# Kernel tuning notes

Measured on AMD Instinct MI355X. Metric: run time of the kernel, lower is better.

The kernel has to match this reference:

```python
import jax, jax.numpy as jnp
import numpy as np

BL = 512
Q_DIM = K_DIM = V_DIM = 512
R = 2
C = Q_DIM // R  # 256


def setup_inputs() -> dict:
    key = jax.random.key(0)
    ks = jax.random.split(key, 11)
    L = 32768
    x1 = jax.random.normal(ks[0], (1, Q_DIM, L), dtype=jnp.float32)
    x2 = jax.random.normal(ks[1], (1, Q_DIM, L), dtype=jnp.float32)
    mask = jnp.ones((1, 1, L), dtype=jnp.float32)
    s_in = 1.0 / np.sqrt(Q_DIM)
    s_out = 1.0 / np.sqrt(C)
    Wq = jax.random.normal(ks[2], (C, Q_DIM), dtype=jnp.float32) * s_in
    bq = jax.random.normal(ks[3], (C,), dtype=jnp.float32) * 0.01
    Wk = jax.random.normal(ks[4], (C, K_DIM), dtype=jnp.float32) * s_in
    bk = jax.random.normal(ks[5], (C,), dtype=jnp.float32) * 0.01
    Wv = jax.random.normal(ks[6], (C, V_DIM), dtype=jnp.float32) * s_in
    bv = jax.random.normal(ks[7], (C,), dtype=jnp.float32) * 0.01
    Wo = jax.random.normal(ks[8], (V_DIM, C), dtype=jnp.float32) * s_out
    bo = jax.random.normal(ks[9], (V_DIM,), dtype=jnp.float32) * 0.01
    return {"x1": x1, "x2": x2, "mask": mask, "Wq": Wq, "bq": bq,
            "Wk": Wk, "bk": bk, "Wv": Wv, "bv": bv, "Wo": Wo, "bo": bo}


def _sliding_att(x1, mask, Wq, bq, Wk, bk, Wv, bv, Wo, bo):
    bl = BL
    half = bl // 2
    B, _, L = x1.shape  # B == 1 (asserted in original)
    # 1x1 Conv1d projections == per-position matmuls over channels
    q = jnp.einsum('oc,bcl->bol', Wq, x1) + bq[None, :, None]  # (1,C,L)
    k = jnp.einsum('oc,bcl->bol', Wk, x1) + bk[None, :, None]
    v = jnp.einsum('oc,bcl->bol', Wv, x1) + bv[None, :, None]
    c1 = q.shape[1]
    nb = L // bl  # L chosen as multiple of bl; padding branch is a no-op
    pm = mask[:, 0:1, :]  # (1,1,L)
    # query blocks: (nb, C, bl)
    qb = q.reshape(1, c1, nb, bl).transpose(0, 2, 1, 3).reshape(nb, c1, bl)
    # pad K/V/mask with bl//2 zeros each side, gather overlapping windows of width 2*bl
    k_pad = jnp.pad(k, ((0, 0), (0, 0), (half, half)))[0]      # (C, L+bl)
    v_pad = jnp.pad(v, ((0, 0), (0, 0), (half, half)))[0]
    pm_pad = jnp.pad(pm, ((0, 0), (0, 0), (half, half)))[0, 0]  # (L+bl,)
    idx = jnp.arange(nb)[:, None] * bl + jnp.arange(2 * bl)[None, :]  # (nb, 2bl)
    kw = k_pad[:, idx].transpose(1, 0, 2)  # (nb, C, 2bl)
    vw = v_pad[:, idx].transpose(1, 0, 2)  # (nb, C, 2bl)
    pmw = pm_pad[idx][:, None, :]          # (nb, 1, 2bl)
    # banded window mask: query i attends keys j with i <= j < i+bl (in window coords)
    rows = jnp.arange(bl)[:, None]
    cols = jnp.arange(2 * bl)[None, :]
    wmask = ((cols >= rows) & (cols < rows + bl)).astype(x1.dtype)  # (bl, 2bl)
    fmask = wmask[None, :, :] * pmw  # (nb, bl, 2bl)
    scale = 1.0 / np.sqrt(c1)
    energy = jnp.einsum('ncl,ncm->nlm', qb, kw) * scale  # (nb, bl, 2bl)
    attn = jax.nn.softmax(energy + jnp.log(fmask + 1e-6), axis=-1) * fmask
    out = jnp.einsum('ncm,nlm->ncl', vw, attn)  # (nb, C, bl)
    out = jax.nn.relu(out)
    out = jnp.einsum('oc,ncl->nol', Wo, out) + bo[None, :, None]  # (nb, V, bl)
    out = out[None].transpose(0, 2, 1, 3).reshape(1, Wo.shape[0], nb * bl)
    return out[:, :, :L] * pm


def reference(x1, x2, mask, Wq, bq, Wk, bk, Wv, bv, Wo, bo):
    # x2 is accepted by the original forward but unused in self-attention
    return _sliding_att(x1, mask, Wq, bq, Wk, bk, Wv, bv, Wo, bo)
```

## Files before the change

kernel.cpp:

```cpp
#include <hip/hip_runtime.h>
#include <hip/hip_bf16.h>
#include <math.h>

#define L 32768
#define C 256
#define QD 512
#define SCALE (1.0f/16.0f)

typedef __hip_bfloat16 bf16;
typedef short v8s __attribute__((ext_vector_type(8)));
typedef short v4s __attribute__((ext_vector_type(4)));
typedef float v4f __attribute__((ext_vector_type(4)));

__device__ __forceinline__ void ldst16(void* lds, const void* g) {
    __builtin_amdgcn_global_load_lds(
        (const __attribute__((address_space(1))) unsigned int*)g,
        (__attribute__((address_space(3))) unsigned int*)lds, 16, 0, 0);
}
__device__ __forceinline__ short bfbits(float x) {
    bf16 h = __float2bfloat16(x);
    return *reinterpret_cast<short*>(&h);
}

__global__ __launch_bounds__(256) void prep(
    const float* __restrict__ Wq, const float* __restrict__ Wk,
    const float* __restrict__ Wv, const float* __restrict__ bq,
    const float* __restrict__ bk, const float* __restrict__ bv,
    const float* __restrict__ Wo,
    bf16* __restrict__ Wall, bf16* __restrict__ Wob, float* __restrict__ ball)
{
    int i = blockIdx.x * 256 + threadIdx.x;
    if (i < 768*512) {
        int row = i >> 9, idx = i & 511;
        const float* src = row < 256 ? Wq : row < 512 ? Wk : Wv;
        Wall[i] = __float2bfloat16(src[(row & 255) * 512 + idx]);
    } else if (i < 768*512 + 512*256) {
        int j = i - 768*512;
        Wob[j] = __float2bfloat16(Wo[j]);
    } else if (i < 768*512 + 512*256 + 768) {
        int j = i - 768*512 - 512*256;
        ball[j] = j < 256 ? bq[j] : j < 512 ? bk[j - 256] : bv[j - 512];
    }
}

__global__ __launch_bounds__(256) void convt(
    const float* __restrict__ x, short* __restrict__ xT)
{
    __shared__ short st[64*72];
    const int t = threadIdx.x;
    const int l0 = blockIdx.x * 64, c0 = blockIdx.y * 64;
    #pragma unroll
    for (int i = 0; i < 2; i++) {
        int v = i*256 + t;
        int c = v >> 3, l8 = (v & 7) << 3;
        const float* p = x + (size_t)(c0 + c) * L + l0 + l8;
        float4 f0 = *(const float4*)p;
        float4 f1 = *(const float4*)(p + 4);
        bf16* stb = (bf16*)st;
        stb[(l8+0)*72 + c] = __float2bfloat16(f0.x);
        stb[(l8+1)*72 + c] = __float2bfloat16(f0.y);
        stb[(l8+2)*72 + c] = __float2bfloat16(f0.z);
        stb[(l8+3)*72 + c] = __float2bfloat16(f0.w);
        stb[(l8+4)*72 + c] = __float2bfloat16(f1.x);
        stb[(l8+5)*72 + c] = __float2bfloat16(f1.y);
        stb[(l8+6)*72 + c] = __float2bfloat16(f1.z);
        stb[(l8+7)*72 + c] = __float2bfloat16(f1.w);
    }
    __syncthreads();
    #pragma unroll
    for (int i = 0; i < 2; i++) {
        int v = i*256 + t;
        int l = v >> 3, c8 = (v & 7) << 3;
        *(v8s*)(xT + (size_t)(l0 + l) * QD + c0 + c8) = *(const v8s*)&st[l*72 + c8];
    }
}

__global__ __launch_bounds__(256) void qkv_gemm(
    const bf16* __restrict__ A, const bf16* __restrict__ B,
    const float* __restrict__ ball,
    bf16* __restrict__ qT, bf16* __restrict__ kT, bf16* __restrict__ vB)
{
    __shared__ short sA[128*32];
    __shared__ short sB[128*32];
    __shared__ short sE[128*136];

    const int t    = threadIdx.x;
    const int lane = t & 63;
    const int w    = t >> 6;
    const int wm   = w & 1, wn = w >> 1;
    const int col  = lane & 15, quad = lane >> 4;
    const int n0   = blockIdx.x * 128;
    const int my   = blockIdx.y;
    const int m0   = my * 128;

    v4f acc[4][4];
    #pragma unroll
    for (int i = 0; i < 4; i++)
        #pragma unroll
        for (int j = 0; j < 4; j++) acc[i][j] = (v4f){0.f,0.f,0.f,0.f};

    for (int k0 = 0; k0 < QD; k0 += 32) {
        #pragma unroll
        for (int j = 0; j < 2; j++) {
            int idx = j*256 + t;
            int m = idx >> 2, k8 = (idx & 3) << 3;
            ldst16(&sA[idx*8], A + (size_t)(m0 + m) * QD + k0 + k8);
        }
        #pragma unroll
        for (int j = 0; j < 2; j++) {
            int idx = j*256 + t;
            int n = idx >> 2, k8 = (idx & 3) << 3;
            ldst16(&sB[idx*8], B + (size_t)(n0 + n) * QD + k0 + k8);
        }
        __syncthreads();
        v8s af[4], bf[4];
        #pragma unroll
        for (int mt = 0; mt < 4; mt++)
            af[mt] = *(const v8s*)&sA[(wm*64 + mt*16 + col)*32 + quad*8];
        #pragma unroll
        for (int nt = 0; nt < 4; nt++)
            bf[nt] = *(const v8s*)&sB[(wn*64 + nt*16 + col)*32 + quad*8];
        #pragma unroll
        for (int mt = 0; mt < 4; mt++)
            #pragma unroll
            for (int nt = 0; nt < 4; nt++)
                acc[mt][nt] = __builtin_amdgcn_mfma_f32_16x16x32_bf16(af[mt], bf[nt], acc[mt][nt], 0, 0, 0);
        __syncthreads();
    }

    float bias_v[4][4];
    #pragma unroll
    for (int mt = 0; mt < 4; mt++)
        #pragma unroll
        for (int r = 0; r < 4; r++)
            bias_v[mt][r] = ball[m0 + wm*64 + mt*16 + quad*4 + r];

    bf16* sEb = (bf16*)sE;
    if (my < 4) {
        #pragma unroll
        for (int mt = 0; mt < 4; mt++)
            #pragma unroll
            for (int nt = 0; nt < 4; nt++)
                #pragma unroll
                for (int r = 0; r < 4; r++)
                    sEb[(wn*64 + nt*16 + col)*136 + wm*64 + mt*16 + quad*4 + r] =
                        __float2bfloat16(acc[mt][nt][r] + bias_v[mt][r]);
        __syncthreads();
        bf16* dst = (my < 2) ? qT : kT;
        const int c0 = (my & 1) * 128;
        #pragma unroll
        for (int j = 0; j < 8; j++) {
            int idx = j*256 + t;
            int n = idx >> 4, c8 = (idx & 15) << 3;
            *(v8s*)(dst + (size_t)(n0 + n) * C + c0 + c8) = *(const v8s*)&sE[n*136 + c8];
        }
    } else {
        #pragma unroll
        for (int mt = 0; mt < 4; mt++)
            #pragma unroll
            for (int nt = 0; nt < 4; nt++)
                #pragma unroll
                for (int r = 0; r < 4; r++)
                    sEb[(wm*64 + mt*16 + quad*4 + r)*136 + wn*64 + nt*16 + col] =
                        __float2bfloat16(acc[mt][nt][r] + bias_v[mt][r]);
        __syncthreads();
        const int c0 = (my - 4) * 128;
        #pragma unroll
        for (int j = 0; j < 8; j++) {
            int idx = j*256 + t;
            int m = idx >> 4, n8 = (idx & 15) << 3;
            *(v8s*)(vB + (size_t)(c0 + m) * L + n0 + n8) = *(const v8s*)&sE[m*136 + n8];
        }
    }
}

__global__ __launch_bounds__(256) void out_gemm(
    const bf16* __restrict__ A, const bf16* __restrict__ B,
    const float* __restrict__ bo, const float* __restrict__ mask,
    float* __restrict__ out)
{
    __shared__ short sA[128*32];
    __shared__ short sB[128*32];
    __shared__ float sEf[64*132];

    const int t    = threadIdx.x;
    const int lane = t & 63;
    const int w    = t >> 6;
    const int wm   = w & 1, wn = w >> 1;
    const int col  = lane & 15, quad = lane >> 4;
    const int n0   = blockIdx.x * 128;
    const int m0   = blockIdx.y * 128;

    v4f acc[4][4];
    #pragma unroll
    for (int i = 0; i < 4; i++)
        #pragma unroll
        for (int j = 0; j < 4; j++) acc[i][j] = (v4f){0.f,0.f,0.f,0.f};

    for (int k0 = 0; k0 < C; k0 += 32) {
        #pragma unroll
        for (int j = 0; j < 2; j++) {
            int idx = j*256 + t;
            int m = idx >> 2, k8 = (idx & 3) << 3;
            ldst16(&sA[idx*8], A + (size_t)(m0 + m) * C + k0 + k8);
        }
        #pragma unroll
        for (int j = 0; j < 2; j++) {
            int idx = j*256 + t;
            int n = idx >> 2, k8 = (idx & 3) << 3;
            ldst16(&sB[idx*8], B + (size_t)(n0 + n) * C + k0 + k8);
        }
        __syncthreads();
        v8s af[4], bf[4];
        #pragma unroll
        for (int mt = 0; mt < 4; mt++)
            af[mt] = *(const v8s*)&sA[(wm*64 + mt*16 + col)*32 + quad*8];
        #pragma unroll
        for (int nt = 0; nt < 4; nt++)
            bf[nt] = *(const v8s*)&sB[(wn*64 + nt*16 + col)*32 + quad*8];
        #pragma unroll
        for (int mt = 0; mt < 4; mt++)
            #pragma unroll
            for (int nt = 0; nt < 4; nt++)
                acc[mt][nt] = __builtin_amdgcn_mfma_f32_16x16x32_bf16(af[mt], bf[nt], acc[mt][nt], 0, 0, 0);
        __syncthreads();
    }

    #pragma unroll
    for (int half = 0; half < 2; half++) {
        if (wm == half) {
            #pragma unroll
            for (int mt = 0; mt < 4; mt++) {
                #pragma unroll
                for (int r = 0; r < 4; r++) {
                    float bb = bo[m0 + half*64 + mt*16 + quad*4 + r];
                    #pragma unroll
                    for (int nt = 0; nt < 4; nt++)
                        sEf[(mt*16 + quad*4 + r)*132 + wn*64 + nt*16 + col] =
                            acc[mt][nt][r] + bb;
                }
            }
        }
        __syncthreads();
        #pragma unroll
        for (int j = 0; j < 8; j++) {
            int idx = j*256 + t;
            int row = idx >> 5, s4 = (idx & 31) << 2;
            float4 vv = *(const float4*)&sEf[row*132 + s4];
            float4 mk = *(const float4*)&mask[n0 + s4];
            vv.x *= mk.x; vv.y *= mk.y; vv.z *= mk.z; vv.w *= mk.w;
            *(float4*)&out[(size_t)(m0 + half*64 + row) * L + n0 + s4] = vv;
        }
        __syncthreads();
    }
}

__device__ __forceinline__ void load_chunk(
    const short* __restrict__ kT, const short* __restrict__ vB,
    int a0, int t, v8s kreg[4], v8s vreg[4])
{
    #pragma unroll
    for (int j = 0; j < 4; j++) {
        int idx = j*512 + t;
        int r = idx >> 5, s = idx & 31;
        int a = min(max(a0 + r, 0), L - 1);
        kreg[j] = *(const v8s*)(kT + (size_t)a * C + s*8);
    }
    #pragma unroll
    for (int j = 0; j < 4; j++) {
        int idx = j*512 + t;
        int c = idx >> 3, s = idx & 7;
        int ab = min(max(a0 + s*8, 0), L - 8);
        vreg[j] = *(const v8s*)(vB + (size_t)c * L + ab);
    }
}

__device__ __forceinline__ void store_chunk(
    short* __restrict__ sK, short* __restrict__ sVt, int t,
    const v8s kreg[4], const v8s vreg[4])
{
    #pragma unroll
    for (int j = 0; j < 4; j++) {
        int idx = j*512 + t;
        int r = idx >> 5, s = idx & 31;
        *(v8s*)&sK[r*264 + s*8] = kreg[j];
    }
    #pragma unroll
    for (int j = 0; j < 4; j++) {
        int idx = j*512 + t;
        int c = idx >> 3, s = idx & 7;
        *(v8s*)&sVt[c*72 + s*8] = vreg[j];
    }
}

__global__ __launch_bounds__(512, 1) void attn_mfma(
    const bf16* __restrict__ qT, const bf16* __restrict__ kT,
    const bf16* __restrict__ vB, const float* __restrict__ mask,
    bf16* __restrict__ aoT)
{
    __shared__ short sK [2][64*264];
    __shared__ short sVt[2][256*72];
    __shared__ short sP [8][16*72];

    const int t    = threadIdx.x;
    const int w    = t >> 6;
    const int lane = t & 63;
    const int col  = lane & 15;
    const int quad = lane >> 4;
    const int bx   = blockIdx.x;
    const int tile = ((bx & 7) << 5) | (bx >> 3);
    const int p0   = tile * 128;
    const int abase = p0 - 256;

    v8s qf[8];
    {
        const short* qp = (const short*)qT + (size_t)(p0 + w*16 + col) * C + quad*8;
        #pragma unroll
        for (int ks = 0; ks < 8; ks++) qf[ks] = *(const v8s*)(qp + ks*32);
    }

    v4f oacc[16];
    #pragma unroll
    for (int i = 0; i < 16; i++) oacc[i] = (v4f){0.f, 0.f, 0.f, 0.f};
    float mrow[4] = {-1e30f, -1e30f, -1e30f, -1e30f};
    float lrow[4] = {0.f, 0.f, 0.f, 0.f};

    const short* kTs = (const short*)kT;
    const short* vBs = (const short*)vB;
    bf16* sPw  = (bf16*)sP[w];
    const short* sPws = (const short*)sP[w];

    v8s kreg[4], vreg[4];
    load_chunk(kTs, vBs, abase, t, kreg, vreg);
    store_chunk(sK[0], sVt[0], t, kreg, vreg);
    __syncthreads();

    for (int ch = 0; ch < 10; ch++) {
        const int a0  = abase + ch*64;
        const int cur = ch & 1;
        const bool pf = (ch < 9);
        if (pf)
            load_chunk(kTs, vBs, a0 + 64, t, kreg, vreg);

        v4f e[4];
        #pragma unroll
        for (int nt = 0; nt < 4; nt++) {
            v4f acc = {0.f, 0.f, 0.f, 0.f};
            const short* kp = &sK[cur][(nt*16 + col)*264 + quad*8];
            #pragma unroll
            for (int ks = 0; ks < 8; ks++) {
                v8s bfrag = *(const v8s*)(kp + ks*32);
                acc = __builtin_amdgcn_mfma_f32_16x16x32_bf16(qf[ks], bfrag, acc, 0, 0, 0);
            }
            e[nt] = acc;
        }

        float cmax[4] = {-1e30f, -1e30f, -1e30f, -1e30f};
        #pragma unroll
        for (int nt = 0; nt < 4; nt++) {
            int a  = a0 + nt*16 + col;
            int aa = ch*64 + nt*16 + col;
            float mval = (a >= 0 && a < L) ? mask[a] : 0.f;
            #pragma unroll
            for (int r = 0; r < 4; r++) {
                int rel = aa - (w*16 + quad*4 + r);
                bool valid = ((unsigned)rel < 512u) && (mval > 0.f);
                float ev = valid ? e[nt][r] * SCALE : -1e30f;
                e[nt][r] = ev;
                cmax[r] = fmaxf(cmax[r], ev);
            }
        }
        #pragma unroll
        for (int off = 1; off < 16; off <<= 1) {
            #pragma unroll
            for (int r = 0; r < 4; r++)
                cmax[r] = fmaxf(cmax[r], __shfl_xor(cmax[r], off));
        }

        float alpha[4];
        #pragma unroll
        for (int r = 0; r < 4; r++) {
            float mnew = fmaxf(mrow[r], cmax[r]);
            alpha[r] = __expf(mrow[r] - mnew);
            mrow[r] = mnew;
        }

        float psum[4] = {0.f, 0.f, 0.f, 0.f};
        #pragma unroll
        for (int nt = 0; nt < 4; nt++) {
            #pragma unroll
            for (int r = 0; r < 4; r++) {
                float ev = e[nt][r];
                float p = (ev > -9e29f) ? __expf(ev - mrow[r]) : 0.f;
                psum[r] += p;
                sPw[(quad*4 + r)*72 + nt*16 + col] = __float2bfloat16(p);
            }
        }
        #pragma unroll
        for (int off = 1; off < 16; off <<= 1) {
            #pragma unroll
            for (int r = 0; r < 4; r++)
                psum[r] += __shfl_xor(psum[r], off);
        }
        #pragma unroll
        for (int r = 0; r < 4; r++) lrow[r] = lrow[r]*alpha[r] + psum[r];

        {
            int src = (col >> 2) << 4;
            float a0b = __shfl(alpha[0], src);
            float a1b = __shfl(alpha[1], src);
            float a2b = __shfl(alpha[2], src);
            float a3b = __shfl(alpha[3], src);
            int rr = col & 3;
            float aO = (rr == 0) ? a0b : (rr == 1) ? a1b : (rr == 2) ? a2b : a3b;
            #pragma unroll
            for (int i = 0; i < 16; i++) {
                oacc[i][0] *= aO; oacc[i][1] *= aO;
                oacc[i][2] *= aO; oacc[i][3] *= aO;
            }
        }

        {
            v8s pf0 = *(const v8s*)&sPws[col*72 + quad*8];
            v8s pf1 = *(const v8s*)&sPws[col*72 + quad*8 + 32];
            #pragma unroll
            for (int ct = 0; ct < 16; ct++) {
                const short* vp = &sVt[cur][(ct*16 + col)*72 + quad*8];
                v8s vf0 = *(const v8s*)vp;
                v8s vf1 = *(const v8s*)(vp + 32);
                oacc[ct] = __builtin_amdgcn_mfma_f32_16x16x32_bf16(vf0, pf0, oacc[ct], 0, 0, 0);
                oacc[ct] = __builtin_amdgcn_mfma_f32_16x16x32_bf16(vf1, pf1, oacc[ct], 0, 0, 0);
            }
        }

        if (pf) {
            store_chunk(sK[cur ^ 1], sVt[cur ^ 1], t, kreg, vreg);
            __syncthreads();
        }
    }

    {
        int src = (col >> 2) << 4;
        float l0b = __shfl(lrow[0], src);
        float l1b = __shfl(lrow[1], src);
        float l2b = __shfl(lrow[2], src);
        float l3b = __shfl(lrow[3], src);
        int rr = col & 3;
        float lO = (rr == 0) ? l0b : (rr == 1) ? l1b : (rr == 2) ? l2b : l3b;
        float inv = (lO > 0.f) ? 1.f / lO : 0.f;
        const int qg = p0 + w*16 + col;
        short* aorow = (short*)aoT + (size_t)qg * C;
        #pragma unroll
        for (int ct = 0; ct < 16; ct++) {
            v4s pk;
            #pragma unroll
            for (int r = 0; r < 4; r++)
                pk[r] = bfbits(fmaxf(oacc[ct][r] * inv, 0.f));
            *(v4s*)(aorow + ct*16 + quad*4) = pk;
        }
    }
}

extern "C" void kernel_launch(void* const* d_in, const int* in_sizes, int n_in,
                              void* d_out, int out_size, void* d_ws, size_t ws_size,
                              hipStream_t stream)
{
    const float* x1   = (const float*)d_in[0];
    const float* mask = (const float*)d_in[2];
    const float* Wq   = (const float*)d_in[3];
    const float* bq   = (const float*)d_in[4];
    const float* Wk   = (const float*)d_in[5];
    const float* bk   = (const float*)d_in[6];
    const float* Wv   = (const float*)d_in[7];
    const float* bv   = (const float*)d_in[8];
    const float* Wo   = (const float*)d_in[9];
    const float* bo   = (const float*)d_in[10];
    float* out = (float*)d_out;

    bf16* x1T  = (bf16*)d_ws;
    bf16* Wall = x1T + (size_t)L * QD;
    bf16* Wob  = Wall + 768*512;
    float* ball = (float*)(Wob + 512*256);
    bf16* qT   = (bf16*)(ball + 768);
    bf16* kT   = qT + (size_t)L * C;
    bf16* vB   = kT + (size_t)L * C;
    bf16* aoT  = vB + (size_t)L * C;

    dim3 blk(256);
    prep<<<dim3((768*512 + 512*256 + 768 + 255)/256), blk, 0, stream>>>(
        Wq, Wk, Wv, bq, bk, bv, Wo, Wall, Wob, ball);
    convt<<<dim3(L/64, QD/64), blk, 0, stream>>>(x1, (short*)x1T);
    qkv_gemm<<<dim3(L/128, 6), blk, 0, stream>>>(Wall, x1T, ball, qT, kT, vB);
    attn_mfma<<<dim3(L/128), dim3(512), 0, stream>>>(qT, kT, vB, mask, aoT);
    out_gemm<<<dim3(L/128, 4), blk, 0, stream>>>(Wob, aoT, bo, mask, out);
}
```

Measured before the change: 292.7 us.

## Transpose QK^T so probabilities stay in registers and drop LDS double buffering

Swaps the MFMA operand order so each lane holds one query column, which puts the softmax row statistics in a single scalar per lane. The bf16 probabilities are then fed straight from registers into 16x16x16 MFMAs for the PV product, with no shared-memory P staging. The K/V double buffer and its register prefetch are replaced by a single buffer loaded synchronously between two barriers. This frees LDS and registers so the launch bound can target 4 blocks per CU. The cost is that global loads are no longer overlapped with compute inside a block, so latency hiding depends on the other resident blocks.

```diff
diff --git a/kernel.cpp b/kernel.cpp
--- a/kernel.cpp
+++ b/kernel.cpp
@@ -20,6 +20,10 @@
 __device__ __forceinline__ short bfbits(float x) {
     bf16 h = __float2bfloat16(x);
     return *reinterpret_cast<short*>(&h);
+}
+__device__ __forceinline__ v4f mfma16(v4s a, v4s b, v4f c) {
+    asm("v_mfma_f32_16x16x16_bf16 %0, %1, %2, %0" : "+v"(c) : "v"(a), "v"(b));
+    return c;
 }
 
 __global__ __launch_bounds__(256) void prep(
@@ -255,52 +259,47 @@
     }
 }
 
-__device__ __forceinline__ void load_chunk(
+__device__ __forceinline__ void relay_chunk(
     const short* __restrict__ kT, const short* __restrict__ vB,
-    int a0, int t, v8s kreg[4], v8s vreg[4])
-{
+    int a0, int t, short* __restrict__ sK, short* __restrict__ sVt)
+{
+    v8s kr[4];
     #pragma unroll
     for (int j = 0; j < 4; j++) {
         int idx = j*512 + t;
         int r = idx >> 5, s = idx & 31;
         int a = min(max(a0 + r, 0), L - 1);
-        kreg[j] = *(const v8s*)(kT + (size_t)a * C + s*8);
-    }
+        kr[j] = *(const v8s*)(kT + (size_t)a * C + s*8);
+    }
+    #pragma unroll
+    for (int j = 0; j < 4; j++) {
+        int idx = j*512 + t;
+        int r = idx >> 5, s = idx & 31;
+        *(v8s*)&sK[r*264 + s*8] = kr[j];
+    }
+    v8s vr[4];
     #pragma unroll
     for (int j = 0; j < 4; j++) {
         int idx = j*512 + t;
         int c = idx >> 3, s = idx & 7;
         int ab = min(max(a0 + s*8, 0), L - 8);
-        vreg[j] = *(const v8s*)(vB + (size_t)c * L + ab);
-    }
-}
-
-__device__ __forceinline__ void store_chunk(
-    short* __restrict__ sK, short* __restrict__ sVt, int t,
-    const v8s kreg[4], const v8s vreg[4])
-{
-    #pragma unroll
-    for (int j = 0; j < 4; j++) {
-        int idx = j*512 + t;
-        int r = idx >> 5, s = idx & 31;
-        *(v8s*)&sK[r*264 + s*8] = kreg[j];
+        vr[j] = *(const v8s*)(vB + (size_t)c * L + ab);
     }
     #pragma unroll
     for (int j = 0; j < 4; j++) {
         int idx = j*512 + t;
         int c = idx >> 3, s = idx & 7;
-        *(v8s*)&sVt[c*72 + s*8] = vreg[j];
-    }
-}
-
-__global__ __launch_bounds__(512, 1) void attn_mfma(
+        *(v8s*)&sVt[c*72 + s*8] = vr[j];
+    }
+}
+
+__global__ __launch_bounds__(512, 4) void attn_mfma(
     const bf16* __restrict__ qT, const bf16* __restrict__ kT,
     const bf16* __restrict__ vB, const float* __restrict__ mask,
     bf16* __restrict__ aoT)
 {
-    __shared__ short sK [2][64*264];
-    __shared__ short sVt[2][256*72];
-    __shared__ short sP [8][16*72];
+    __shared__ short sK [64*264];
+    __shared__ short sVt[256*72];
 
     const int t    = threadIdx.x;
     const int w    = t >> 6;
@@ -311,10 +310,11 @@
     const int tile = ((bx & 7) << 5) | (bx >> 3);
     const int p0   = tile * 128;
     const int abase = p0 - 256;
+    const int qrow = w*16 + col;
 
     v8s qf[8];
     {
-        const short* qp = (const short*)qT + (size_t)(p0 + w*16 + col) * C + quad*8;
+        const short* qp = (const short*)qT + (size_t)(p0 + qrow) * C + quad*8;
         #pragma unroll
         for (int ks = 0; ks < 8; ks++) qf[ks] = *(const v8s*)(qp + ks*32);
     }
@@ -322,142 +322,104 @@
     v4f oacc[16];
     #pragma unroll
     for (int i = 0; i < 16; i++) oacc[i] = (v4f){0.f, 0.f, 0.f, 0.f};
-    float mrow[4] = {-1e30f, -1e30f, -1e30f, -1e30f};
-    float lrow[4] = {0.f, 0.f, 0.f, 0.f};
+    float mrow = -1e30f, lrow = 0.f;
 
     const short* kTs = (const short*)kT;
     const short* vBs = (const short*)vB;
-    bf16* sPw  = (bf16*)sP[w];
-    const short* sPws = (const short*)sP[w];
-
-    v8s kreg[4], vreg[4];
-    load_chunk(kTs, vBs, abase, t, kreg, vreg);
-    store_chunk(sK[0], sVt[0], t, kreg, vreg);
+
+    relay_chunk(kTs, vBs, abase, t, sK, sVt);
     __syncthreads();
 
     for (int ch = 0; ch < 10; ch++) {
-        const int a0  = abase + ch*64;
-        const int cur = ch & 1;
-        const bool pf = (ch < 9);
-        if (pf)
-            load_chunk(kTs, vBs, a0 + 64, t, kreg, vreg);
+        const int a0 = abase + ch*64;
 
         v4f e[4];
         #pragma unroll
         for (int nt = 0; nt < 4; nt++) {
             v4f acc = {0.f, 0.f, 0.f, 0.f};
-            const short* kp = &sK[cur][(nt*16 + col)*264 + quad*8];
+            const short* kp = &sK[(nt*16 + col)*264 + quad*8];
             #pragma unroll
             for (int ks = 0; ks < 8; ks++) {
-                v8s bfrag = *(const v8s*)(kp + ks*32);
-                acc = __builtin_amdgcn_mfma_f32_16x16x32_bf16(qf[ks], bfrag, acc, 0, 0, 0);
+                v8s af = *(const v8s*)(kp + ks*32);
+                acc = __builtin_amdgcn_mfma_f32_16x16x32_bf16(af, qf[ks], acc, 0, 0, 0);
             }
             e[nt] = acc;
         }
 
-        float cmax[4] = {-1e30f, -1e30f, -1e30f, -1e30f};
+        float cmax = -1e30f;
         #pragma unroll
         for (int nt = 0; nt < 4; nt++) {
-            int a  = a0 + nt*16 + col;
-            int aa = ch*64 + nt*16 + col;
-            float mval = (a >= 0 && a < L) ? mask[a] : 0.f;
+            int kc = nt*16 + quad*4;
+            int a  = a0 + kc;
+            int ac = min(max(a, 0), L - 4);
+            float4 m4 = *(const float4*)&mask[ac];
+            float mv[4] = {m4.x, m4.y, m4.z, m4.w};
             #pragma unroll
             for (int r = 0; r < 4; r++) {
-                int rel = aa - (w*16 + quad*4 + r);
-                bool valid = ((unsigned)rel < 512u) && (mval > 0.f);
+                int rel = ch*64 + kc + r - qrow;
+                bool valid = ((unsigned)rel < 512u) &&
+                             ((unsigned)(a + r) < (unsigned)L) && (mv[r] > 0.f);
                 float ev = valid ? e[nt][r] * SCALE : -1e30f;
                 e[nt][r] = ev;
-                cmax[r] = fmaxf(cmax[r], ev);
+                cmax = fmaxf(cmax, ev);
             }
         }
-        #pragma unroll
-        for (int off = 1; off < 16; off <<= 1) {
-            #pragma unroll
-            for (int r = 0; r < 4; r++)
-                cmax[r] = fmaxf(cmax[r], __shfl_xor(cmax[r], off));
-        }
-
-        float alpha[4];
-        #pragma unroll
-        for (int r = 0; r < 4; r++) {
-            float mnew = fmaxf(mrow[r], cmax[r]);
-            alpha[r] = __expf(mrow[r] - mnew);
-            mrow[r] = mnew;
-        }
-
-        float psum[4] = {0.f, 0.f, 0.f, 0.f};
+        cmax = fmaxf(cmax, __shfl_xor(cmax, 16));
+        cmax = fmaxf(cmax, __shfl_xor(cmax, 32));
+
+        float mnew  = fmaxf(mrow, cmax);
+        float alpha = __expf(mrow - mnew);
+        mrow = mnew;
+
+        float psum = 0.f;
+        v4s pfr[4];
         #pragma unroll
         for (int nt = 0; nt < 4; nt++) {
             #pragma unroll
             for (int r = 0; r < 4; r++) {
                 float ev = e[nt][r];
-                float p = (ev > -9e29f) ? __expf(ev - mrow[r]) : 0.f;
-                psum[r] += p;
-                sPw[(quad*4 + r)*72 + nt*16 + col] = __float2bfloat16(p);
+                float p  = (ev > -9e29f) ? __expf(ev - mrow) : 0.f;
+                psum += p;
+                pfr[nt][r] = bfbits(p);
             }
         }
-        #pragma unroll
-        for (int off = 1; off < 16; off <<= 1) {
-            #pragma unroll
-            for (int r = 0; r < 4; r++)
-                psum[r] += __shfl_xor(psum[r], off);
-        }
-        #pragma unroll
-        for (int r = 0; r < 4; r++) lrow[r] = lrow[r]*alpha[r] + psum[r];
-
-        {
-            int src = (col >> 2) << 4;
-            float a0b = __shfl(alpha[0], src);
-            float a1b = __shfl(alpha[1], src);
-            float a2b = __shfl(alpha[2], src);
-            float a3b = __shfl(alpha[3], src);
-            int rr = col & 3;
-            float aO = (rr == 0) ? a0b : (rr == 1) ? a1b : (rr == 2) ? a2b : a3b;
-            #pragma unroll
-            for (int i = 0; i < 16; i++) {
-                oacc[i][0] *= aO; oacc[i][1] *= aO;
-                oacc[i][2] *= aO; oacc[i][3] *= aO;
+        psum += __shfl_xor(psum, 16);
+        psum += __shfl_xor(psum, 32);
+        lrow = lrow * alpha + psum;
+
+        #pragma unroll
+        for (int i = 0; i < 16; i++) {
+            oacc[i][0] *= alpha; oacc[i][1] *= alpha;
+            oacc[i][2] *= alpha; oacc[i][3] *= alpha;
+        }
+
+        #pragma unroll
+        for (int ct = 0; ct < 16; ct++) {
+            const short* vp = &sVt[(ct*16 + col)*72 + quad*4];
+            #pragma unroll
+            for (int nt = 0; nt < 4; nt++) {
+                v4s vf = *(const v4s*)(vp + nt*16);
+                oacc[ct] = mfma16(vf, pfr[nt], oacc[ct]);
             }
         }
 
-        {
-            v8s pf0 = *(const v8s*)&sPws[col*72 + quad*8];
-            v8s pf1 = *(const v8s*)&sPws[col*72 + quad*8 + 32];
-            #pragma unroll
-            for (int ct = 0; ct < 16; ct++) {
-                const short* vp = &sVt[cur][(ct*16 + col)*72 + quad*8];
-                v8s vf0 = *(const v8s*)vp;
-                v8s vf1 = *(const v8s*)(vp + 32);
-                oacc[ct] = __builtin_amdgcn_mfma_f32_16x16x32_bf16(vf0, pf0, oacc[ct], 0, 0, 0);
-                oacc[ct] = __builtin_amdgcn_mfma_f32_16x16x32_bf16(vf1, pf1, oacc[ct], 0, 0, 0);
-            }
-        }
-
-        if (pf) {
-            store_chunk(sK[cur ^ 1], sVt[cur ^ 1], t, kreg, vreg);
+        if (ch < 9) {
             __syncthreads();
-        }
-    }
-
-    {
-        int src = (col >> 2) << 4;
-        float l0b = __shfl(lrow[0], src);
-        float l1b = __shfl(lrow[1], src);
-        float l2b = __shfl(lrow[2], src);
-        float l3b = __shfl(lrow[3], src);
-        int rr = col & 3;
-        float lO = (rr == 0) ? l0b : (rr == 1) ? l1b : (rr == 2) ? l2b : l3b;
-        float inv = (lO > 0.f) ? 1.f / lO : 0.f;
-        const int qg = p0 + w*16 + col;
-        short* aorow = (short*)aoT + (size_t)qg * C;
-        #pragma unroll
-        for (int ct = 0; ct < 16; ct++) {
-            v4s pk;
-            #pragma unroll
-            for (int r = 0; r < 4; r++)
-                pk[r] = bfbits(fmaxf(oacc[ct][r] * inv, 0.f));
-            *(v4s*)(aorow + ct*16 + quad*4) = pk;
-        }
+            relay_chunk(kTs, vBs, a0 + 64, t, sK, sVt);
+            __syncthreads();
+        }
+    }
+
+    float inv = (lrow > 0.f) ? 1.f / lrow : 0.f;
+    const int qg = p0 + qrow;
+    short* aorow = (short*)aoT + (size_t)qg * C;
+    #pragma unroll
+    for (int ct = 0; ct < 16; ct++) {
+        v4s pk;
+        #pragma unroll
+        for (int r = 0; r < 4; r++)
+            pk[r] = bfbits(fmaxf(oacc[ct][r] * inv, 0.f));
+        *(v4s*)(aorow + ct*16 + quad*4) = pk;
     }
 }
 
```

Result: slower. 380.2 us (+29.9%).
